# Performance work log

Hardware: AMD Instinct MI355X
Metric: run time of the kernel (lower is better)

Reference implementation:

```python
import jax, jax.numpy as jnp
import numpy as np

NBATCH, NSAMPLES, DIM, NHID, NLAYERS, DEG = 8, 2048, 4, 64, 3, 16
N = NBATCH * NSAMPLES
E = N * DEG
EPS = 1e-5


def setup_inputs() -> dict:
    key = jax.random.key(0)
    ks = jax.random.split(key, 16)
    x = jax.random.uniform(ks[0], (N, DIM), dtype=jnp.float32)
    # within-graph random edges (emulating radius_graph with contiguous batch)
    gid = jnp.repeat(jnp.arange(NBATCH, dtype=jnp.int64), NSAMPLES * DEG)
    src = jax.random.randint(ks[1], (E,), 0, NSAMPLES).astype(jnp.int64) + gid * NSAMPLES
    tgt = jax.random.randint(ks[2], (E,), 0, NSAMPLES).astype(jnp.int64) + gid * NSAMPLES
    edge_index = jnp.stack([src, tgt], axis=0)
    s = 0.05
    inp = {
        'x': x,
        'edge_index': edge_index,
        'enc_w': jax.random.normal(ks[3], (DIM, NHID), jnp.float32) * s,
        'enc_b': jnp.zeros((NHID,), jnp.float32),
        'm1_w': jax.random.normal(ks[4], (NLAYERS, 2 * NHID, NHID), jnp.float32) * s,
        'm1_b': jnp.zeros((NLAYERS, NHID), jnp.float32),
        'm2_w': jax.random.normal(ks[5], (NLAYERS, NHID, NHID), jnp.float32) * s,
        'm2_b': jnp.zeros((NLAYERS, NHID), jnp.float32),
        'u1_w': jax.random.normal(ks[6], (NLAYERS, NHID + NHID, NHID), jnp.float32) * s,
        'u1_b': jnp.zeros((NLAYERS, NHID), jnp.float32),
        'u2_w': jax.random.normal(ks[7], (NLAYERS, NHID, NHID), jnp.float32) * s,
        'u2_b': jnp.zeros((NLAYERS, NHID), jnp.float32),
        'dec_w': jax.random.normal(ks[8], (NHID, DIM), jnp.float32) * s,
        'dec_b': jnp.zeros((DIM,), jnp.float32),
    }
    return inp


def _l2star_sq(X):
    # Warnock formula for squared L2-star discrepancy, per graph.
    # X: [B, n, d] in [0,1]
    n = X.shape[1]
    d = X.shape[2]
    t1 = (1.0 / 3.0) ** d
    prod1 = jnp.prod(1.0 - X * X, axis=-1)          # [B, n]
    t2 = prod1.sum(axis=-1) * (2.0 / (n * (2.0 ** d)))
    # pairwise prod_k (1 - max(x_ik, x_jk)); loop over small d to avoid [B,n,n,d]
    acc = jnp.ones((X.shape[0], n, n), X.dtype)
    for k in range(d):
        acc = acc * (1.0 - jnp.maximum(X[:, :, None, k], X[:, None, :, k]))
    t3 = acc.sum(axis=(-1, -2)) / (n * n)
    return t1 - t2 + t3  # [B]


def _forward(x, edge_index, enc_w, enc_b, m1_w, m1_b, m2_w, m2_b,
             u1_w, u1_b, u2_w, u2_b, dec_w, dec_b):
    src, tgt = edge_index[0], edge_index[1]
    h = x @ enc_w + enc_b  # [N, NHID]
    for l in range(NLAYERS):
        x_j = h[src]  # source features
        x_i = h[tgt]  # target features
        m = jax.nn.relu(jnp.concatenate([x_i, x_j], axis=-1) @ m1_w[l] + m1_b[l])
        m = jax.nn.relu(m @ m2_w[l] + m2_b[l])
        agg = jax.ops.segment_sum(m, tgt, num_segments=N)  # default aggr='add'
        h = jax.nn.relu(jnp.concatenate([h, agg], axis=-1) @ u1_w[l] + u1_b[l])
        h = jax.nn.relu(h @ u2_w[l] + u2_b[l])
        # InstanceNorm per graph (batch is contiguous blocks of NSAMPLES)
        hb = h.reshape(NBATCH, NSAMPLES, NHID)
        mean = hb.mean(axis=1, keepdims=True)
        var = hb.var(axis=1, keepdims=True)
        h = ((hb - mean) * jax.lax.rsqrt(var + EPS)).reshape(N, NHID)
    X = jax.nn.sigmoid(h @ dec_w + dec_b).reshape(NBATCH, NSAMPLES, DIM)
    loss = jnp.mean(_l2star_sq(X))
    return loss, X


def reference(x, edge_index, enc_w, enc_b, m1_w, m1_b, m2_w, m2_b,
              u1_w, u1_b, u2_w, u2_b, dec_w, dec_b):
    return _forward(x, edge_index, enc_w, enc_b, m1_w, m1_b, m2_w, m2_b,
                    u1_w, u1_b, u2_w, u2_b, dec_w, dec_b)
```

## Files before the change

### kernel.cpp

```cpp
#include <hip/hip_runtime.h>
#include <hip/hip_fp16.h>
#include <math.h>

#define NB 8
#define NS 2048
#define NN (NB*NS)
#define NE (NN*16)
#define EPSF 1e-5f

typedef float  f32x4 __attribute__((ext_vector_type(4)));
typedef _Float16 f16x8 __attribute__((ext_vector_type(8)));
union F8 { f16x8 v; unsigned u[4]; };

__device__ __forceinline__ unsigned pk2h(float a, float b) {
    __half2 hh = __floats2half2_rn(a, b);
    unsigned u; __builtin_memcpy(&u, &hh, 4); return u;
}

__global__ __launch_bounds__(256) void k_init(int* __restrict__ deg,
                                              float* __restrict__ acc)
{
    int i = blockIdx.x*256 + threadIdx.x;
    if (i < NN) deg[i] = 0;
    if (i < 4) acc[i] = 0.f;
}

__global__ __launch_bounds__(256) void k_pre0M(
    const float* __restrict__ x,
    const float* __restrict__ encW, const float* __restrict__ encB,
    float* __restrict__ h,
    const float* __restrict__ W1, const float* __restrict__ B1,
    float* __restrict__ A, float* __restrict__ Bm,
    float* __restrict__ gz,
    const int* __restrict__ srcv, const int* __restrict__ tgtv,
    int* __restrict__ deg, int* __restrict__ ssrc)
{
    alignas(16) __shared__ _Float16 sWp[8192];
    __shared__ float sEw[256], sEb[64];
    {
        int gid = blockIdx.x*256 + threadIdx.x;
        #pragma unroll
        for (int it = 0; it < 4; it++) {
            int e = gid + it*65536;
            int t = tgtv[e];
            int pos = atomicAdd(&deg[t], 1) & 63;
            ssrc[t*64 + pos] = srcv[e];
        }
    }
    for (int idx = threadIdx.x; idx < 8192; idx += 256) {
        int k = idx >> 7, n = idx & 127;
        float val = (n < 64) ? W1[k*64 + n] : W1[(64+k)*64 + (n-64)];
        int ks = k >> 5, qd = (k >> 3) & 3, j = k & 7, nt = n >> 4, cl = n & 15;
        sWp[(((ks*8+nt)*4+qd)*16+cl)*8 + j] = (_Float16)val;
    }
    sEw[threadIdx.x] = encW[threadIdx.x];
    if (threadIdx.x < 64) sEb[threadIdx.x] = encB[threadIdx.x];
    if (blockIdx.x == 0)
        for (int i = threadIdx.x; i < 2*NB*64; i += 256) gz[i] = 0.f;
    __syncthreads();
    const int lane = threadIdx.x & 63;
    const int wv = threadIdx.x >> 6;
    const int col = lane & 15, quad = lane >> 4;
    const int n0w = blockIdx.x*64 + wv*16;
    const int n = n0w + col;
    float4 x4 = *(const float4*)&x[(size_t)n*4];
    float xv[16];
    #pragma unroll
    for (int hh = 0; hh < 2; hh++)
        #pragma unroll
        for (int j = 0; j < 8; j++) {
            int f = hh*32 + quad*8 + j;
            float v = sEb[f];
            v = fmaf(x4.x, sEw[f],     v);
            v = fmaf(x4.y, sEw[64+f],  v);
            v = fmaf(x4.z, sEw[128+f], v);
            v = fmaf(x4.w, sEw[192+f], v);
            xv[hh*8+j] = v;
        }
    float* hp = &h[(size_t)n*64 + quad*8];
    *(float4*)&hp[0]  = *(float4*)&xv[0];
    *(float4*)&hp[4]  = *(float4*)&xv[4];
    *(float4*)&hp[32] = *(float4*)&xv[8];
    *(float4*)&hp[36] = *(float4*)&xv[12];
    F8 af0, af1;
    af0.u[0] = pk2h(xv[0],  xv[1]);  af0.u[1] = pk2h(xv[2],  xv[3]);
    af0.u[2] = pk2h(xv[4],  xv[5]);  af0.u[3] = pk2h(xv[6],  xv[7]);
    af1.u[0] = pk2h(xv[8],  xv[9]);  af1.u[1] = pk2h(xv[10], xv[11]);
    af1.u[2] = pk2h(xv[12], xv[13]); af1.u[3] = pk2h(xv[14], xv[15]);
    float b1v[4];
    #pragma unroll
    for (int nt = 0; nt < 4; nt++) b1v[nt] = B1[nt*16+col];
    #pragma unroll
    for (int nt = 0; nt < 8; nt++) {
        f32x4 acc = {0.f,0.f,0.f,0.f};
        F8 bf; bf.v = *(const f16x8*)&sWp[(((0*8+nt)*4+quad)*16+col)*8];
        acc = __builtin_amdgcn_mfma_f32_16x16x32_f16(af0.v, bf.v, acc, 0, 0, 0);
        bf.v = *(const f16x8*)&sWp[(((1*8+nt)*4+quad)*16+col)*8];
        acc = __builtin_amdgcn_mfma_f32_16x16x32_f16(af1.v, bf.v, acc, 0, 0, 0);
        if (nt < 4) {
            float bb = b1v[nt];
            A[(size_t)(n0w + quad*4 + 0)*64 + nt*16 + col] = acc.x + bb;
            A[(size_t)(n0w + quad*4 + 1)*64 + nt*16 + col] = acc.y + bb;
            A[(size_t)(n0w + quad*4 + 2)*64 + nt*16 + col] = acc.z + bb;
            A[(size_t)(n0w + quad*4 + 3)*64 + nt*16 + col] = acc.w + bb;
        } else {
            Bm[(size_t)(n0w + quad*4 + 0)*64 + (nt-4)*16 + col] = acc.x;
            Bm[(size_t)(n0w + quad*4 + 1)*64 + (nt-4)*16 + col] = acc.y;
            Bm[(size_t)(n0w + quad*4 + 2)*64 + (nt-4)*16 + col] = acc.z;
            Bm[(size_t)(n0w + quad*4 + 3)*64 + (nt-4)*16 + col] = acc.w;
        }
    }
}

__global__ __launch_bounds__(256) void k_edge4(
    const float* __restrict__ A, const float* __restrict__ Bm,
    const int* __restrict__ deg, const int* __restrict__ ssrc,
    const float* __restrict__ W2, const float* __restrict__ B2,
    float* __restrict__ agg)
{
    __shared__ float sW[64*64];
    for (int i = threadIdx.x; i < 64*64; i += 256) sW[i] = W2[i];
    __syncthreads();
    const int lane = threadIdx.x & 63;
    const int col = lane & 15, quad = lane >> 4;
    F8 bf[4][2];
    #pragma unroll
    for (int nt = 0; nt < 4; nt++)
        #pragma unroll
        for (int ks = 0; ks < 2; ks++)
            #pragma unroll
            for (int jj = 0; jj < 4; jj++) {
                int k = ks*32 + quad*8 + jj*2;
                bf[nt][ks].u[jj] = pk2h(sW[k*64 + nt*16 + col],
                                        sW[(k+1)*64 + nt*16 + col]);
            }
    float b2v[4];
    #pragma unroll
    for (int nt = 0; nt < 4; nt++) b2v[nt] = B2[nt*16 + col];

    const int wid = blockIdx.x*4 + (threadIdx.x >> 6);
    const int nwv = gridDim.x*4;
    for (int t = wid; t < NN; t += nwv) {
        int cnt = deg[t]; if (cnt > 64) cnt = 64;
        int base = t*64;
        const float* ar = &A[(size_t)t*64 + quad*8];
        float4 a0 = *(const float4*)&ar[0];
        float4 a1 = *(const float4*)&ar[4];
        float4 a2 = *(const float4*)&ar[32];
        float4 a3 = *(const float4*)&ar[36];
        float cs[4] = {0.f, 0.f, 0.f, 0.f};
        for (int s0 = 0; s0 < cnt; s0 += 16) {
            int v = cnt - s0;
            int cc = col < v-1 ? col : v-1;
            int sr = ssrc[base + s0 + cc];
            const float* br = &Bm[(size_t)sr*64 + quad*8];
            float4 b0 = *(const float4*)&br[0];
            float4 b1 = *(const float4*)&br[4];
            float4 b2_ = *(const float4*)&br[32];
            float4 b3 = *(const float4*)&br[36];
            F8 af0, af1;
            af0.u[0] = pk2h(fmaxf(a0.x+b0.x,0.f), fmaxf(a0.y+b0.y,0.f));
            af0.u[1] = pk2h(fmaxf(a0.z+b0.z,0.f), fmaxf(a0.w+b0.w,0.f));
            af0.u[2] = pk2h(fmaxf(a1.x+b1.x,0.f), fmaxf(a1.y+b1.y,0.f));
            af0.u[3] = pk2h(fmaxf(a1.z+b1.z,0.f), fmaxf(a1.w+b1.w,0.f));
            af1.u[0] = pk2h(fmaxf(a2.x+b2_.x,0.f), fmaxf(a2.y+b2_.y,0.f));
            af1.u[1] = pk2h(fmaxf(a2.z+b2_.z,0.f), fmaxf(a2.w+b2_.w,0.f));
            af1.u[2] = pk2h(fmaxf(a3.x+b3.x,0.f), fmaxf(a3.y+b3.y,0.f));
            af1.u[3] = pk2h(fmaxf(a3.z+b3.z,0.f), fmaxf(a3.w+b3.w,0.f));
            #pragma unroll
            for (int nt = 0; nt < 4; nt++) {
                f32x4 acc = __builtin_amdgcn_mfma_f32_16x16x32_f16(
                                af0.v, bf[nt][0].v, (f32x4){0.f,0.f,0.f,0.f}, 0, 0, 0);
                acc = __builtin_amdgcn_mfma_f32_16x16x32_f16(
                                af1.v, bf[nt][1].v, acc, 0, 0, 0);
                float r0 = (quad*4+0 < v) ? fmaxf(acc.x + b2v[nt], 0.f) : 0.f;
                float r1 = (quad*4+1 < v) ? fmaxf(acc.y + b2v[nt], 0.f) : 0.f;
                float r2 = (quad*4+2 < v) ? fmaxf(acc.z + b2v[nt], 0.f) : 0.f;
                float r3 = (quad*4+3 < v) ? fmaxf(acc.w + b2v[nt], 0.f) : 0.f;
                cs[nt] += (r0 + r1) + (r2 + r3);
            }
        }
        #pragma unroll
        for (int nt = 0; nt < 4; nt++) {
            float vv = cs[nt];
            vv += __shfl_down(vv, 32, 64);
            vv += __shfl_down(vv, 16, 64);
            cs[nt] = vv;
        }
        if (lane < 16) {
            agg[(size_t)t*64 +  0 + lane] = cs[0];
            agg[(size_t)t*64 + 16 + lane] = cs[1];
            agg[(size_t)t*64 + 32 + lane] = cs[2];
            agg[(size_t)t*64 + 48 + lane] = cs[3];
        }
    }
}

__global__ __launch_bounds__(256) void k_updateM(
    float* __restrict__ h, const float* __restrict__ agg,
    const float* __restrict__ W1, const float* __restrict__ B1,
    const float* __restrict__ W2, const float* __restrict__ B2,
    float* __restrict__ gout)
{
    alignas(16) __shared__ _Float16 sW1u[8192];
    alignas(16) __shared__ _Float16 sW2u[4096];
    alignas(16) __shared__ float sHid[4][16*68];
    __shared__ float sSum[4][64], sSq[4][64];
    for (int idx = threadIdx.x; idx < 8192; idx += 256) {
        int k = idx >> 6, n = idx & 63;
        int ks = k >> 5, qd = (k >> 3) & 3, j = k & 7, nt = n >> 4, cl = n & 15;
        sW1u[(((ks*4+nt)*4+qd)*16+cl)*8 + j] = (_Float16)W1[idx];
    }
    for (int idx = threadIdx.x; idx < 4096; idx += 256) {
        int k = idx >> 6, n = idx & 63;
        int ks = k >> 5, qd = (k >> 3) & 3, j = k & 7, nt = n >> 4, cl = n & 15;
        sW2u[(((ks*4+nt)*4+qd)*16+cl)*8 + j] = (_Float16)W2[idx];
    }
    __syncthreads();
    const int lane = threadIdx.x & 63;
    const int wv = threadIdx.x >> 6;
    const int col = lane & 15, quad = lane >> 4;
    const int n0w = blockIdx.x*64 + wv*16;
    const float* hp = &h[(size_t)(n0w+col)*64 + quad*8];
    const float* ap = &agg[(size_t)(n0w+col)*64 + quad*8];
    float4 h0 = *(const float4*)&hp[0];
    float4 h1 = *(const float4*)&hp[4];
    float4 h2 = *(const float4*)&hp[32];
    float4 h3 = *(const float4*)&hp[36];
    float4 g0 = *(const float4*)&ap[0];
    float4 g1 = *(const float4*)&ap[4];
    float4 g2 = *(const float4*)&ap[32];
    float4 g3 = *(const float4*)&ap[36];
    F8 af[4];
    af[0].u[0] = pk2h(h0.x, h0.y); af[0].u[1] = pk2h(h0.z, h0.w);
    af[0].u[2] = pk2h(h1.x, h1.y); af[0].u[3] = pk2h(h1.z, h1.w);
    af[1].u[0] = pk2h(h2.x, h2.y); af[1].u[1] = pk2h(h2.z, h2.w);
    af[1].u[2] = pk2h(h3.x, h3.y); af[1].u[3] = pk2h(h3.z, h3.w);
    af[2].u[0] = pk2h(g0.x, g0.y); af[2].u[1] = pk2h(g0.z, g0.w);
    af[2].u[2] = pk2h(g1.x, g1.y); af[2].u[3] = pk2h(g1.z, g1.w);
    af[3].u[0] = pk2h(g2.x, g2.y); af[3].u[1] = pk2h(g2.z, g2.w);
    af[3].u[2] = pk2h(g3.x, g3.y); af[3].u[3] = pk2h(g3.z, g3.w);
    float b1v[4], b2v[4];
    #pragma unroll
    for (int nt = 0; nt < 4; nt++) { b1v[nt] = B1[nt*16+col]; b2v[nt] = B2[nt*16+col]; }
    float* hid = &sHid[wv][0];
    #pragma unroll
    for (int nt = 0; nt < 4; nt++) {
        f32x4 acc = {0.f,0.f,0.f,0.f};
        #pragma unroll
        for (int ks = 0; ks < 4; ks++) {
            F8 bf; bf.v = *(const f16x8*)&sW1u[(((ks*4+nt)*4+quad)*16+col)*8];
            acc = __builtin_amdgcn_mfma_f32_16x16x32_f16(af[ks].v, bf.v, acc, 0, 0, 0);
        }
        hid[(quad*4+0)*68 + nt*16+col] = fmaxf(acc.x + b1v[nt], 0.f);
        hid[(quad*4+1)*68 + nt*16+col] = fmaxf(acc.y + b1v[nt], 0.f);
        hid[(quad*4+2)*68 + nt*16+col] = fmaxf(acc.z + b1v[nt], 0.f);
        hid[(quad*4+3)*68 + nt*16+col] = fmaxf(acc.w + b1v[nt], 0.f);
    }
    __syncthreads();
    const float* hr = &hid[col*68 + quad*8];
    float4 q0 = *(const float4*)&hr[0];
    float4 q1 = *(const float4*)&hr[4];
    float4 q2 = *(const float4*)&hr[32];
    float4 q3 = *(const float4*)&hr[36];
    F8 e0, e1;
    e0.u[0] = pk2h(q0.x, q0.y); e0.u[1] = pk2h(q0.z, q0.w);
    e0.u[2] = pk2h(q1.x, q1.y); e0.u[3] = pk2h(q1.z, q1.w);
    e1.u[0] = pk2h(q2.x, q2.y); e1.u[1] = pk2h(q2.z, q2.w);
    e1.u[2] = pk2h(q3.x, q3.y); e1.u[3] = pk2h(q3.z, q3.w);
    float ss[4], sq[4];
    #pragma unroll
    for (int nt = 0; nt < 4; nt++) {
        f32x4 acc = {0.f,0.f,0.f,0.f};
        F8 bf; bf.v = *(const f16x8*)&sW2u[(((0*4+nt)*4+quad)*16+col)*8];
        acc = __builtin_amdgcn_mfma_f32_16x16x32_f16(e0.v, bf.v, acc, 0, 0, 0);
        bf.v = *(const f16x8*)&sW2u[(((1*4+nt)*4+quad)*16+col)*8];
        acc = __builtin_amdgcn_mfma_f32_16x16x32_f16(e1.v, bf.v, acc, 0, 0, 0);
        float o0 = fmaxf(acc.x + b2v[nt], 0.f);
        float o1 = fmaxf(acc.y + b2v[nt], 0.f);
        float o2 = fmaxf(acc.z + b2v[nt], 0.f);
        float o3 = fmaxf(acc.w + b2v[nt], 0.f);
        h[(size_t)(n0w + quad*4 + 0)*64 + nt*16 + col] = o0;
        h[(size_t)(n0w + quad*4 + 1)*64 + nt*16 + col] = o1;
        h[(size_t)(n0w + quad*4 + 2)*64 + nt*16 + col] = o2;
        h[(size_t)(n0w + quad*4 + 3)*64 + nt*16 + col] = o3;
        ss[nt] = (o0 + o1) + (o2 + o3);
        sq[nt] = (o0*o0 + o1*o1) + (o2*o2 + o3*o3);
    }
    #pragma unroll
    for (int nt = 0; nt < 4; nt++) {
        float v = ss[nt];
        v += __shfl_down(v, 32, 64); v += __shfl_down(v, 16, 64);
        float w2 = sq[nt];
        w2 += __shfl_down(w2, 32, 64); w2 += __shfl_down(w2, 16, 64);
        if (lane < 16) { sSum[wv][nt*16+lane] = v; sSq[wv][nt*16+lane] = w2; }
    }
    __syncthreads();
    if (threadIdx.x < 128) {
        int ch = threadIdx.x & 63, hf = threadIdx.x >> 6;
        int b = (int)(blockIdx.x >> 5);
        if (hf == 0) {
            float t_ = sSum[0][ch]+sSum[1][ch]+sSum[2][ch]+sSum[3][ch];
            atomicAdd(&gout[b*64 + ch], t_);
        } else {
            float t_ = sSq[0][ch]+sSq[1][ch]+sSq[2][ch]+sSq[3][ch];
            atomicAdd(&gout[NB*64 + b*64 + ch], t_);
        }
    }
}

__global__ __launch_bounds__(256) void k_preM(
    float* __restrict__ h,
    const float* __restrict__ W1, const float* __restrict__ B1,
    float* __restrict__ A, float* __restrict__ Bm,
    const float* __restrict__ gin, float* __restrict__ gz)
{
    alignas(16) __shared__ _Float16 sWp[8192];
    __shared__ float sMean[64], sRstd[64];
    for (int idx = threadIdx.x; idx < 8192; idx += 256) {
        int k = idx >> 7, n = idx & 127;
        float val = (n < 64) ? W1[k*64 + n] : W1[(64+k)*64 + (n-64)];
        int ks = k >> 5, qd = (k >> 3) & 3, j = k & 7, nt = n >> 4, cl = n & 15;
        sWp[(((ks*8+nt)*4+qd)*16+cl)*8 + j] = (_Float16)val;
    }
    if (threadIdx.x < 64) {
        int b = (int)(blockIdx.x >> 5);
        float s  = gin[b*64 + threadIdx.x];
        float qq = gin[NB*64 + b*64 + threadIdx.x];
        float mean = s * (1.f/NS);
        float var  = qq * (1.f/NS) - mean*mean;
        sMean[threadIdx.x] = mean;
        sRstd[threadIdx.x] = rsqrtf(var + EPSF);
    }
    if (blockIdx.x == 0)
        for (int i = threadIdx.x; i < 2*NB*64; i += 256) gz[i] = 0.f;
    __syncthreads();
    const int lane = threadIdx.x & 63;
    const int wv = threadIdx.x >> 6;
    const int col = lane & 15, quad = lane >> 4;
    const int n0w = blockIdx.x*64 + wv*16;
    float* hp = &h[(size_t)(n0w+col)*64 + quad*8];
    float xv[16];
    *(float4*)&xv[0]  = *(const float4*)&hp[0];
    *(float4*)&xv[4]  = *(const float4*)&hp[4];
    *(float4*)&xv[8]  = *(const float4*)&hp[32];
    *(float4*)&xv[12] = *(const float4*)&hp[36];
    #pragma unroll
    for (int t2 = 0; t2 < 8; t2++) {
        int f = quad*8 + t2;
        xv[t2] = (xv[t2] - sMean[f]) * sRstd[f];
    }
    #pragma unroll
    for (int t2 = 0; t2 < 8; t2++) {
        int f = 32 + quad*8 + t2;
        xv[8+t2] = (xv[8+t2] - sMean[f]) * sRstd[f];
    }
    *(float4*)&hp[0]  = *(float4*)&xv[0];
    *(float4*)&hp[4]  = *(float4*)&xv[4];
    *(float4*)&hp[32] = *(float4*)&xv[8];
    *(float4*)&hp[36] = *(float4*)&xv[12];
    F8 af0, af1;
    af0.u[0] = pk2h(xv[0],  xv[1]);  af0.u[1] = pk2h(xv[2],  xv[3]);
    af0.u[2] = pk2h(xv[4],  xv[5]);  af0.u[3] = pk2h(xv[6],  xv[7]);
    af1.u[0] = pk2h(xv[8],  xv[9]);  af1.u[1] = pk2h(xv[10], xv[11]);
    af1.u[2] = pk2h(xv[12], xv[13]); af1.u[3] = pk2h(xv[14], xv[15]);
    float b1v[4];
    #pragma unroll
    for (int nt = 0; nt < 4; nt++) b1v[nt] = B1[nt*16+col];
    #pragma unroll
    for (int nt = 0; nt < 8; nt++) {
        f32x4 acc = {0.f,0.f,0.f,0.f};
        F8 bf; bf.v = *(const f16x8*)&sWp[(((0*8+nt)*4+quad)*16+col)*8];
        acc = __builtin_amdgcn_mfma_f32_16x16x32_f16(af0.v, bf.v, acc, 0, 0, 0);
        bf.v = *(const f16x8*)&sWp[(((1*8+nt)*4+quad)*16+col)*8];
        acc = __builtin_amdgcn_mfma_f32_16x16x32_f16(af1.v, bf.v, acc, 0, 0, 0);
        if (nt < 4) {
            float bb = b1v[nt];
            A[(size_t)(n0w + quad*4 + 0)*64 + nt*16 + col] = acc.x + bb;
            A[(size_t)(n0w + quad*4 + 1)*64 + nt*16 + col] = acc.y + bb;
            A[(size_t)(n0w + quad*4 + 2)*64 + nt*16 + col] = acc.z + bb;
            A[(size_t)(n0w + quad*4 + 3)*64 + nt*16 + col] = acc.w + bb;
        } else {
            Bm[(size_t)(n0w + quad*4 + 0)*64 + (nt-4)*16 + col] = acc.x;
            Bm[(size_t)(n0w + quad*4 + 1)*64 + (nt-4)*16 + col] = acc.y;
            Bm[(size_t)(n0w + quad*4 + 2)*64 + (nt-4)*16 + col] = acc.z;
            Bm[(size_t)(n0w + quad*4 + 3)*64 + (nt-4)*16 + col] = acc.w;
        }
    }
}

__global__ __launch_bounds__(256) void k_dec(
    const float* __restrict__ h, const float* __restrict__ Wd, const float* __restrict__ bd,
    const float* __restrict__ g, float* __restrict__ xbuf, float* __restrict__ out1,
    float* __restrict__ accum)
{
    int n = blockIdx.x*256 + threadIdx.x;
    int b = n >> 11;
    __shared__ float sM[64], sR[64];
    __shared__ float sWd[256];
    if (threadIdx.x < 64) {
        float s  = g[b*64 + threadIdx.x];
        float qq = g[NB*64 + b*64 + threadIdx.x];
        float mean = s * (1.f/NS);
        float var  = qq * (1.f/NS) - mean*mean;
        sM[threadIdx.x] = mean; sR[threadIdx.x] = rsqrtf(var + EPSF);
    }
    for (int i = threadIdx.x; i < 256; i += 256) sWd[i] = Wd[i];
    __syncthreads();
    float a0 = bd[0], a1 = bd[1], a2 = bd[2], a3 = bd[3];
    const float* hr = h + (size_t)n*64;
    #pragma unroll 8
    for (int k = 0; k < 64; k++) {
        float v = (hr[k] - sM[k]) * sR[k];
        a0 = fmaf(v, sWd[k*4+0], a0);
        a1 = fmaf(v, sWd[k*4+1], a1);
        a2 = fmaf(v, sWd[k*4+2], a2);
        a3 = fmaf(v, sWd[k*4+3], a3);
    }
    float4 o;
    o.x = 1.f/(1.f + expf(-a0));
    o.y = 1.f/(1.f + expf(-a1));
    o.z = 1.f/(1.f + expf(-a2));
    o.w = 1.f/(1.f + expf(-a3));
    *(float4*)&xbuf[(size_t)n*4] = o;
    out1[n*4+0] = o.x; out1[n*4+1] = o.y; out1[n*4+2] = o.z; out1[n*4+3] = o.w;
    float p = (1.f-o.x*o.x)*(1.f-o.y*o.y)*(1.f-o.z*o.z)*(1.f-o.w*o.w);
    for (int offs = 32; offs; offs >>= 1) p += __shfl_down(p, offs, 64);
    __shared__ float ws[4];
    if ((threadIdx.x & 63) == 0) ws[threadIdx.x >> 6] = p;
    __syncthreads();
    if (threadIdx.x == 0) atomicAdd(&accum[0], ws[0]+ws[1]+ws[2]+ws[3]);
}

__global__ __launch_bounds__(256) void k_t3(const float* __restrict__ X,
                                            float* __restrict__ accum,
                                            float* __restrict__ out)
{
    int b = blockIdx.x >> 5, c = blockIdx.x & 31;
    __shared__ float sX[NS*4];
    const float* Xb = X + (size_t)b*NS*4;
    for (int idx = threadIdx.x; idx < NS*4; idx += 256) sX[idx] = Xb[idx];
    __syncthreads();
    const float4* sX4 = (const float4*)sX;
    int il = threadIdx.x & 63, wv = threadIdx.x >> 6;
    float4 xi = sX4[c*64 + il];
    float acc = 0.f;
    #pragma unroll 4
    for (int s = 0; s < 512; s++) {
        float4 xj = sX4[wv*512 + s];
        acc += (1.f - fmaxf(xi.x, xj.x)) * (1.f - fmaxf(xi.y, xj.y))
             * (1.f - fmaxf(xi.z, xj.z)) * (1.f - fmaxf(xi.w, xj.w));
    }
    for (int offs = 32; offs; offs >>= 1) acc += __shfl_down(acc, offs, 64);
    __shared__ float ws[4];
    if (il == 0) ws[wv] = acc;
    __syncthreads();
    if (threadIdx.x == 0) {
        atomicAdd(&accum[1], ws[0]+ws[1]+ws[2]+ws[3]);
        __threadfence();
        unsigned t = atomicAdd((unsigned int*)&accum[2], 1u);
        if (t == (unsigned)(NB*32 - 1)) {
            float A2 = __hip_atomic_load(&accum[0], __ATOMIC_ACQUIRE, __HIP_MEMORY_SCOPE_AGENT);
            float A3 = __hip_atomic_load(&accum[1], __ATOMIC_ACQUIRE, __HIP_MEMORY_SCOPE_AGENT);
            float t1 = 1.f/81.f;
            float t2 = (2.f/(NS*16.f)) * (A2 / NB);
            float t3 = (A3 / ((float)NS*(float)NS)) / NB;
            out[0] = t1 - t2 + t3;
        }
    }
}

extern "C" void kernel_launch(void* const* d_in, const int* in_sizes, int n_in,
                              void* d_out, int out_size, void* d_ws, size_t ws_size,
                              hipStream_t stream)
{
    const float* x     = (const float*)d_in[0];
    const int*   ei    = (const int*)d_in[1];
    const float* enc_w = (const float*)d_in[2];
    const float* enc_b = (const float*)d_in[3];
    const float* m1w   = (const float*)d_in[4];
    const float* m1b   = (const float*)d_in[5];
    const float* m2w   = (const float*)d_in[6];
    const float* m2b   = (const float*)d_in[7];
    const float* u1w   = (const float*)d_in[8];
    const float* u1b   = (const float*)d_in[9];
    const float* u2w   = (const float*)d_in[10];
    const float* u2b   = (const float*)d_in[11];
    const float* dw    = (const float*)d_in[12];
    const float* db    = (const float*)d_in[13];
    float* out = (float*)d_out;

    float* h    = (float*)d_ws;
    float* agg  = h    + NN*64;
    float* Apre = agg  + NN*64;
    float* Bpre = Apre + NN*64;
    float* g0   = Bpre + NN*64;
    float* g1   = g0   + 2*NB*64;
    float* acc  = g1   + 2*NB*64;
    int*   deg  = (int*)(acc + 4);
    int*   ssrc = deg + NN;
    float* xbuf = Apre;

    const int* srcv = ei;
    const int* tgtv = ei + NE;
    float* gbuf[2] = {g0, g1};

    k_init<<<NN/256, 256, 0, stream>>>(deg, acc);
    k_pre0M<<<NN/64, 256, 0, stream>>>(x, enc_w, enc_b, h, m1w, m1b,
                                       Apre, Bpre, g0, srcv, tgtv, deg, ssrc);

    for (int l = 0; l < 3; l++) {
        if (l)
            k_preM<<<NN/64, 256, 0, stream>>>(h, m1w + l*128*64, m1b + l*64,
                                              Apre, Bpre,
                                              gbuf[(l+1)&1], gbuf[l&1]);
        k_edge4<<<1024, 256, 0, stream>>>(Apre, Bpre, deg, ssrc,
                                          m2w + l*64*64, m2b + l*64, agg);
        k_updateM<<<NN/64, 256, 0, stream>>>(h, agg,
                                             u1w + l*128*64, u1b + l*64,
                                             u2w + l*64*64,  u2b + l*64,
                                             gbuf[l&1]);
    }

    k_dec<<<NN/256, 256, 0, stream>>>(h, dw, db, g0, xbuf, out + 1, acc);
    k_t3<<<NB*32, 256, 0, stream>>>(xbuf, acc, out);
}
```

Before: 241.0 us.

## Fuse edge message kernel with node update kernel via shared-memory aggregation

Merges the per-edge message MLP/aggregation kernel and the node update MLP kernel into one kernel, so each block aggregates 16 target nodes into shared memory and then runs the update MLP on them. This drops the global agg buffer round trip and one launch per layer, and preloads each node's source indices once per wave and distributes them with wave shuffles. In exchange, every block of only 16 nodes (1024 blocks) must convert and stage the full update and message weights into LDS. The update phase also runs on a single wave while the other three sit idle, and there are many more per-graph stat atomics.

```diff
diff --git a/kernel.cpp b/kernel.cpp
--- a/kernel.cpp
+++ b/kernel.cpp
@@ -112,37 +112,56 @@
     }
 }
 
-__global__ __launch_bounds__(256) void k_edge4(
+__global__ __launch_bounds__(256, 4) void k_eu(
     const float* __restrict__ A, const float* __restrict__ Bm,
     const int* __restrict__ deg, const int* __restrict__ ssrc,
-    const float* __restrict__ W2, const float* __restrict__ B2,
-    float* __restrict__ agg)
-{
-    __shared__ float sW[64*64];
-    for (int i = threadIdx.x; i < 64*64; i += 256) sW[i] = W2[i];
+    const float* __restrict__ W2e, const float* __restrict__ B2e,
+    float* __restrict__ h,
+    const float* __restrict__ W1u, const float* __restrict__ B1u,
+    const float* __restrict__ W2u, const float* __restrict__ B2u,
+    float* __restrict__ gout)
+{
+    alignas(16) __shared__ _Float16 sW1u[8192];
+    alignas(16) __shared__ _Float16 sW2u[4096];
+    alignas(16) __shared__ _Float16 sM2[4096];
+    alignas(16) __shared__ float sAgg[16*68];
+    for (int idx = threadIdx.x; idx < 8192; idx += 256) {
+        int k = idx >> 6, n = idx & 63;
+        int ks = k >> 5, qd = (k >> 3) & 3, j = k & 7, nt = n >> 4, cl = n & 15;
+        sW1u[(((ks*4+nt)*4+qd)*16+cl)*8 + j] = (_Float16)W1u[idx];
+    }
+    for (int idx = threadIdx.x; idx < 4096; idx += 256) {
+        int k = idx >> 6, n = idx & 63;
+        int ks = k >> 5, qd = (k >> 3) & 3, j = k & 7, nt = n >> 4, cl = n & 15;
+        sW2u[(((ks*4+nt)*4+qd)*16+cl)*8 + j] = (_Float16)W2u[idx];
+        sM2 [(((ks*4+nt)*4+qd)*16+cl)*8 + j] = (_Float16)W2e[idx];
+    }
     __syncthreads();
     const int lane = threadIdx.x & 63;
+    const int wv = threadIdx.x >> 6;
     const int col = lane & 15, quad = lane >> 4;
-    F8 bf[4][2];
+    F8 bfe[4][2];
     #pragma unroll
     for (int nt = 0; nt < 4; nt++)
         #pragma unroll
         for (int ks = 0; ks < 2; ks++)
-            #pragma unroll
-            for (int jj = 0; jj < 4; jj++) {
-                int k = ks*32 + quad*8 + jj*2;
-                bf[nt][ks].u[jj] = pk2h(sW[k*64 + nt*16 + col],
-                                        sW[(k+1)*64 + nt*16 + col]);
-            }
-    float b2v[4];
-    #pragma unroll
-    for (int nt = 0; nt < 4; nt++) b2v[nt] = B2[nt*16 + col];
-
-    const int wid = blockIdx.x*4 + (threadIdx.x >> 6);
-    const int nwv = gridDim.x*4;
-    for (int t = wid; t < NN; t += nwv) {
-        int cnt = deg[t]; if (cnt > 64) cnt = 64;
-        int base = t*64;
+            bfe[nt][ks].v = *(const f16x8*)&sM2[(((ks*4+nt)*4+quad)*16+col)*8];
+    float b2e[4];
+    #pragma unroll
+    for (int nt = 0; nt < 4; nt++) b2e[nt] = B2e[nt*16 + col];
+
+    const int t_base = blockIdx.x * 16;
+    int cnts[4], sv[4];
+    #pragma unroll
+    for (int m = 0; m < 4; m++) {
+        int t = t_base + wv*4 + m;
+        cnts[m] = deg[t];
+        sv[m] = ssrc[t*64 + lane];
+    }
+    #pragma unroll
+    for (int m = 0; m < 4; m++) {
+        int t = t_base + wv*4 + m;
+        int cnt = cnts[m] > 64 ? 64 : cnts[m];
         const float* ar = &A[(size_t)t*64 + quad*8];
         float4 a0 = *(const float4*)&ar[0];
         float4 a1 = *(const float4*)&ar[4];
@@ -152,7 +171,7 @@
         for (int s0 = 0; s0 < cnt; s0 += 16) {
             int v = cnt - s0;
             int cc = col < v-1 ? col : v-1;
-            int sr = ssrc[base + s0 + cc];
+            int sr = __shfl(sv[m], s0 + cc, 64);
             const float* br = &Bm[(size_t)sr*64 + quad*8];
             float4 b0 = *(const float4*)&br[0];
             float4 b1 = *(const float4*)&br[4];
@@ -170,13 +189,13 @@
             #pragma unroll
             for (int nt = 0; nt < 4; nt++) {
                 f32x4 acc = __builtin_amdgcn_mfma_f32_16x16x32_f16(
-                                af0.v, bf[nt][0].v, (f32x4){0.f,0.f,0.f,0.f}, 0, 0, 0);
+                                af0.v, bfe[nt][0].v, (f32x4){0.f,0.f,0.f,0.f}, 0, 0, 0);
                 acc = __builtin_amdgcn_mfma_f32_16x16x32_f16(
-                                af1.v, bf[nt][1].v, acc, 0, 0, 0);
-                float r0 = (quad*4+0 < v) ? fmaxf(acc.x + b2v[nt], 0.f) : 0.f;
-                float r1 = (quad*4+1 < v) ? fmaxf(acc.y + b2v[nt], 0.f) : 0.f;
-                float r2 = (quad*4+2 < v) ? fmaxf(acc.z + b2v[nt], 0.f) : 0.f;
-                float r3 = (quad*4+3 < v) ? fmaxf(acc.w + b2v[nt], 0.f) : 0.f;
+                                af1.v, bfe[nt][1].v, acc, 0, 0, 0);
+                float r0 = (quad*4+0 < v) ? fmaxf(acc.x + b2e[nt], 0.f) : 0.f;
+                float r1 = (quad*4+1 < v) ? fmaxf(acc.y + b2e[nt], 0.f) : 0.f;
+                float r2 = (quad*4+2 < v) ? fmaxf(acc.z + b2e[nt], 0.f) : 0.f;
+                float r3 = (quad*4+3 < v) ? fmaxf(acc.w + b2e[nt], 0.f) : 0.f;
                 cs[nt] += (r0 + r1) + (r2 + r3);
             }
         }
@@ -188,123 +207,95 @@
             cs[nt] = vv;
         }
         if (lane < 16) {
-            agg[(size_t)t*64 +  0 + lane] = cs[0];
-            agg[(size_t)t*64 + 16 + lane] = cs[1];
-            agg[(size_t)t*64 + 32 + lane] = cs[2];
-            agg[(size_t)t*64 + 48 + lane] = cs[3];
-        }
-    }
-}
-
-__global__ __launch_bounds__(256) void k_updateM(
-    float* __restrict__ h, const float* __restrict__ agg,
-    const float* __restrict__ W1, const float* __restrict__ B1,
-    const float* __restrict__ W2, const float* __restrict__ B2,
-    float* __restrict__ gout)
-{
-    alignas(16) __shared__ _Float16 sW1u[8192];
-    alignas(16) __shared__ _Float16 sW2u[4096];
-    alignas(16) __shared__ float sHid[4][16*68];
-    __shared__ float sSum[4][64], sSq[4][64];
-    for (int idx = threadIdx.x; idx < 8192; idx += 256) {
-        int k = idx >> 6, n = idx & 63;
-        int ks = k >> 5, qd = (k >> 3) & 3, j = k & 7, nt = n >> 4, cl = n & 15;
-        sW1u[(((ks*4+nt)*4+qd)*16+cl)*8 + j] = (_Float16)W1[idx];
-    }
-    for (int idx = threadIdx.x; idx < 4096; idx += 256) {
-        int k = idx >> 6, n = idx & 63;
-        int ks = k >> 5, qd = (k >> 3) & 3, j = k & 7, nt = n >> 4, cl = n & 15;
-        sW2u[(((ks*4+nt)*4+qd)*16+cl)*8 + j] = (_Float16)W2[idx];
-    }
-    __syncthreads();
-    const int lane = threadIdx.x & 63;
-    const int wv = threadIdx.x >> 6;
-    const int col = lane & 15, quad = lane >> 4;
-    const int n0w = blockIdx.x*64 + wv*16;
-    const float* hp = &h[(size_t)(n0w+col)*64 + quad*8];
-    const float* ap = &agg[(size_t)(n0w+col)*64 + quad*8];
-    float4 h0 = *(const float4*)&hp[0];
-    float4 h1 = *(const float4*)&hp[4];
-    float4 h2 = *(const float4*)&hp[32];
-    float4 h3 = *(const float4*)&hp[36];
-    float4 g0 = *(const float4*)&ap[0];
-    float4 g1 = *(const float4*)&ap[4];
-    float4 g2 = *(const float4*)&ap[32];
-    float4 g3 = *(const float4*)&ap[36];
-    F8 af[4];
-    af[0].u[0] = pk2h(h0.x, h0.y); af[0].u[1] = pk2h(h0.z, h0.w);
-    af[0].u[2] = pk2h(h1.x, h1.y); af[0].u[3] = pk2h(h1.z, h1.w);
-    af[1].u[0] = pk2h(h2.x, h2.y); af[1].u[1] = pk2h(h2.z, h2.w);
-    af[1].u[2] = pk2h(h3.x, h3.y); af[1].u[3] = pk2h(h3.z, h3.w);
-    af[2].u[0] = pk2h(g0.x, g0.y); af[2].u[1] = pk2h(g0.z, g0.w);
-    af[2].u[2] = pk2h(g1.x, g1.y); af[2].u[3] = pk2h(g1.z, g1.w);
-    af[3].u[0] = pk2h(g2.x, g2.y); af[3].u[1] = pk2h(g2.z, g2.w);
-    af[3].u[2] = pk2h(g3.x, g3.y); af[3].u[3] = pk2h(g3.z, g3.w);
-    float b1v[4], b2v[4];
-    #pragma unroll
-    for (int nt = 0; nt < 4; nt++) { b1v[nt] = B1[nt*16+col]; b2v[nt] = B2[nt*16+col]; }
-    float* hid = &sHid[wv][0];
-    #pragma unroll
-    for (int nt = 0; nt < 4; nt++) {
-        f32x4 acc = {0.f,0.f,0.f,0.f};
-        #pragma unroll
-        for (int ks = 0; ks < 4; ks++) {
-            F8 bf; bf.v = *(const f16x8*)&sW1u[(((ks*4+nt)*4+quad)*16+col)*8];
-            acc = __builtin_amdgcn_mfma_f32_16x16x32_f16(af[ks].v, bf.v, acc, 0, 0, 0);
-        }
-        hid[(quad*4+0)*68 + nt*16+col] = fmaxf(acc.x + b1v[nt], 0.f);
-        hid[(quad*4+1)*68 + nt*16+col] = fmaxf(acc.y + b1v[nt], 0.f);
-        hid[(quad*4+2)*68 + nt*16+col] = fmaxf(acc.z + b1v[nt], 0.f);
-        hid[(quad*4+3)*68 + nt*16+col] = fmaxf(acc.w + b1v[nt], 0.f);
-    }
-    __syncthreads();
-    const float* hr = &hid[col*68 + quad*8];
-    float4 q0 = *(const float4*)&hr[0];
-    float4 q1 = *(const float4*)&hr[4];
-    float4 q2 = *(const float4*)&hr[32];
-    float4 q3 = *(const float4*)&hr[36];
-    F8 e0, e1;
-    e0.u[0] = pk2h(q0.x, q0.y); e0.u[1] = pk2h(q0.z, q0.w);
-    e0.u[2] = pk2h(q1.x, q1.y); e0.u[3] = pk2h(q1.z, q1.w);
-    e1.u[0] = pk2h(q2.x, q2.y); e1.u[1] = pk2h(q2.z, q2.w);
-    e1.u[2] = pk2h(q3.x, q3.y); e1.u[3] = pk2h(q3.z, q3.w);
-    float ss[4], sq[4];
-    #pragma unroll
-    for (int nt = 0; nt < 4; nt++) {
-        f32x4 acc = {0.f,0.f,0.f,0.f};
-        F8 bf; bf.v = *(const f16x8*)&sW2u[(((0*4+nt)*4+quad)*16+col)*8];
-        acc = __builtin_amdgcn_mfma_f32_16x16x32_f16(e0.v, bf.v, acc, 0, 0, 0);
-        bf.v = *(const f16x8*)&sW2u[(((1*4+nt)*4+quad)*16+col)*8];
-        acc = __builtin_amdgcn_mfma_f32_16x16x32_f16(e1.v, bf.v, acc, 0, 0, 0);
-        float o0 = fmaxf(acc.x + b2v[nt], 0.f);
-        float o1 = fmaxf(acc.y + b2v[nt], 0.f);
-        float o2 = fmaxf(acc.z + b2v[nt], 0.f);
-        float o3 = fmaxf(acc.w + b2v[nt], 0.f);
-        h[(size_t)(n0w + quad*4 + 0)*64 + nt*16 + col] = o0;
-        h[(size_t)(n0w + quad*4 + 1)*64 + nt*16 + col] = o1;
-        h[(size_t)(n0w + quad*4 + 2)*64 + nt*16 + col] = o2;
-        h[(size_t)(n0w + quad*4 + 3)*64 + nt*16 + col] = o3;
-        ss[nt] = (o0 + o1) + (o2 + o3);
-        sq[nt] = (o0*o0 + o1*o1) + (o2*o2 + o3*o3);
-    }
-    #pragma unroll
-    for (int nt = 0; nt < 4; nt++) {
-        float v = ss[nt];
-        v += __shfl_down(v, 32, 64); v += __shfl_down(v, 16, 64);
-        float w2 = sq[nt];
-        w2 += __shfl_down(w2, 32, 64); w2 += __shfl_down(w2, 16, 64);
-        if (lane < 16) { sSum[wv][nt*16+lane] = v; sSq[wv][nt*16+lane] = w2; }
-    }
-    __syncthreads();
-    if (threadIdx.x < 128) {
-        int ch = threadIdx.x & 63, hf = threadIdx.x >> 6;
-        int b = (int)(blockIdx.x >> 5);
-        if (hf == 0) {
-            float t_ = sSum[0][ch]+sSum[1][ch]+sSum[2][ch]+sSum[3][ch];
-            atomicAdd(&gout[b*64 + ch], t_);
-        } else {
-            float t_ = sSq[0][ch]+sSq[1][ch]+sSq[2][ch]+sSq[3][ch];
-            atomicAdd(&gout[NB*64 + b*64 + ch], t_);
+            sAgg[(wv*4+m)*68 +  0 + lane] = cs[0];
+            sAgg[(wv*4+m)*68 + 16 + lane] = cs[1];
+            sAgg[(wv*4+m)*68 + 32 + lane] = cs[2];
+            sAgg[(wv*4+m)*68 + 48 + lane] = cs[3];
+        }
+    }
+    __syncthreads();
+    if (wv == 0) {
+        const int n0w = t_base;
+        const float* hp = &h[(size_t)(n0w+col)*64 + quad*8];
+        float4 h0 = *(const float4*)&hp[0];
+        float4 h1 = *(const float4*)&hp[4];
+        float4 h2 = *(const float4*)&hp[32];
+        float4 h3 = *(const float4*)&hp[36];
+        const float* ap = &sAgg[col*68 + quad*8];
+        float4 g0 = *(const float4*)&ap[0];
+        float4 g1 = *(const float4*)&ap[4];
+        float4 g2 = *(const float4*)&ap[32];
+        float4 g3 = *(const float4*)&ap[36];
+        F8 af[4];
+        af[0].u[0] = pk2h(h0.x, h0.y); af[0].u[1] = pk2h(h0.z, h0.w);
+        af[0].u[2] = pk2h(h1.x, h1.y); af[0].u[3] = pk2h(h1.z, h1.w);
+        af[1].u[0] = pk2h(h2.x, h2.y); af[1].u[1] = pk2h(h2.z, h2.w);
+        af[1].u[2] = pk2h(h3.x, h3.y); af[1].u[3] = pk2h(h3.z, h3.w);
+        af[2].u[0] = pk2h(g0.x, g0.y); af[2].u[1] = pk2h(g0.z, g0.w);
+        af[2].u[2] = pk2h(g1.x, g1.y); af[2].u[3] = pk2h(g1.z, g1.w);
+        af[3].u[0] = pk2h(g2.x, g2.y); af[3].u[1] = pk2h(g2.z, g2.w);
+        af[3].u[2] = pk2h(g3.x, g3.y); af[3].u[3] = pk2h(g3.z, g3.w);
+        float b1v[4], b2v[4];
+        #pragma unroll
+        for (int nt = 0; nt < 4; nt++) { b1v[nt] = B1u[nt*16+col]; b2v[nt] = B2u[nt*16+col]; }
+        #pragma unroll
+        for (int nt = 0; nt < 4; nt++) {
+            f32x4 acc = {0.f,0.f,0.f,0.f};
+            #pragma unroll
+            for (int ks = 0; ks < 4; ks++) {
+                F8 bf; bf.v = *(const f16x8*)&sW1u[(((ks*4+nt)*4+quad)*16+col)*8];
+                acc = __builtin_amdgcn_mfma_f32_16x16x32_f16(af[ks].v, bf.v, acc, 0, 0, 0);
+            }
+            sAgg[(quad*4+0)*68 + nt*16+col] = fmaxf(acc.x + b1v[nt], 0.f);
+            sAgg[(quad*4+1)*68 + nt*16+col] = fmaxf(acc.y + b1v[nt], 0.f);
+            sAgg[(quad*4+2)*68 + nt*16+col] = fmaxf(acc.z + b1v[nt], 0.f);
+            sAgg[(quad*4+3)*68 + nt*16+col] = fmaxf(acc.w + b1v[nt], 0.f);
+        }
+        const float* hr = &sAgg[col*68 + quad*8];
+        float4 q0 = *(const float4*)&hr[0];
+        float4 q1 = *(const float4*)&hr[4];
+        float4 q2 = *(const float4*)&hr[32];
+        float4 q3 = *(const float4*)&hr[36];
+        F8 e0, e1;
+        e0.u[0] = pk2h(q0.x, q0.y); e0.u[1] = pk2h(q0.z, q0.w);
+        e0.u[2] = pk2h(q1.x, q1.y); e0.u[3] = pk2h(q1.z, q1.w);
+        e1.u[0] = pk2h(q2.x, q2.y); e1.u[1] = pk2h(q2.z, q2.w);
+        e1.u[2] = pk2h(q3.x, q3.y); e1.u[3] = pk2h(q3.z, q3.w);
+        float ss[4], sq[4];
+        #pragma unroll
+        for (int nt = 0; nt < 4; nt++) {
+            f32x4 acc = {0.f,0.f,0.f,0.f};
+            F8 bf; bf.v = *(const f16x8*)&sW2u[(((0*4+nt)*4+quad)*16+col)*8];
+            acc = __builtin_amdgcn_mfma_f32_16x16x32_f16(e0.v, bf.v, acc, 0, 0, 0);
+            bf.v = *(const f16x8*)&sW2u[(((1*4+nt)*4+quad)*16+col)*8];
+            acc = __builtin_amdgcn_mfma_f32_16x16x32_f16(e1.v, bf.v, acc, 0, 0, 0);
+            float o0 = fmaxf(acc.x + b2v[nt], 0.f);
+            float o1 = fmaxf(acc.y + b2v[nt], 0.f);
+            float o2 = fmaxf(acc.z + b2v[nt], 0.f);
+            float o3 = fmaxf(acc.w + b2v[nt], 0.f);
+            h[(size_t)(n0w + quad*4 + 0)*64 + nt*16 + col] = o0;
+            h[(size_t)(n0w + quad*4 + 1)*64 + nt*16 + col] = o1;
+            h[(size_t)(n0w + quad*4 + 2)*64 + nt*16 + col] = o2;
+            h[(size_t)(n0w + quad*4 + 3)*64 + nt*16 + col] = o3;
+            ss[nt] = (o0 + o1) + (o2 + o3);
+            sq[nt] = (o0*o0 + o1*o1) + (o2*o2 + o3*o3);
+        }
+        #pragma unroll
+        for (int nt = 0; nt < 4; nt++) {
+            float v = ss[nt];
+            v += __shfl_down(v, 32, 64); v += __shfl_down(v, 16, 64);
+            ss[nt] = v;
+            float w2 = sq[nt];
+            w2 += __shfl_down(w2, 32, 64); w2 += __shfl_down(w2, 16, 64);
+            sq[nt] = w2;
+        }
+        if (lane < 16) {
+            int b = (int)(blockIdx.x >> 7);
+            #pragma unroll
+            for (int nt = 0; nt < 4; nt++) {
+                atomicAdd(&gout[b*64 + nt*16 + lane], ss[nt]);
+                atomicAdd(&gout[NB*64 + b*64 + nt*16 + lane], sq[nt]);
+            }
         }
     }
 }
@@ -491,8 +482,7 @@
     float* out = (float*)d_out;
 
     float* h    = (float*)d_ws;
-    float* agg  = h    + NN*64;
-    float* Apre = agg  + NN*64;
+    float* Apre = h    + NN*64;
     float* Bpre = Apre + NN*64;
     float* g0   = Bpre + NN*64;
     float* g1   = g0   + 2*NB*64;
@@ -514,12 +504,12 @@
             k_preM<<<NN/64, 256, 0, stream>>>(h, m1w + l*128*64, m1b + l*64,
                                               Apre, Bpre,
                                               gbuf[(l+1)&1], gbuf[l&1]);
-        k_edge4<<<1024, 256, 0, stream>>>(Apre, Bpre, deg, ssrc,
-                                          m2w + l*64*64, m2b + l*64, agg);
-        k_updateM<<<NN/64, 256, 0, stream>>>(h, agg,
-                                             u1w + l*128*64, u1b + l*64,
-                                             u2w + l*64*64,  u2b + l*64,
-                                             gbuf[l&1]);
+        k_eu<<<NN/16, 256, 0, stream>>>(Apre, Bpre, deg, ssrc,
+                                        m2w + l*64*64, m2b + l*64,
+                                        h,
+                                        u1w + l*128*64, u1b + l*64,
+                                        u2w + l*64*64,  u2b + l*64,
+                                        gbuf[l&1]);
     }
 
     k_dec<<<NN/256, 256, 0, stream>>>(h, dw, db, g0, xbuf, out + 1, acc);
```

Result: faster. 229.6 us (-4.7%).
